# Kernel optimization log

Hardware: AMD Instinct MI355X
Metric: run time of the kernel (lower is better)

Reference implementation:

```python
import jax, jax.numpy as jnp
import numpy as np

HID, PROJ, ATTN = 512, 1024, 128
B, L = 4, 2048


def _apply_rope(x):
    # x: [B, L, 2, ATTN]; RoPE over sequence dim (axis=1)
    half = x.shape[-1] // 2
    inv_freq = jnp.power(10000.0, -jnp.arange(half, dtype=jnp.float32) / half)
    pos = jnp.arange(x.shape[1], dtype=x.dtype)
    sinusoid = pos[:, None] * inv_freq.astype(x.dtype)          # [L, half]
    sin = jnp.sin(sinusoid)[None, :, None, :]                   # [1, L, 1, half]
    cos = jnp.cos(sinusoid)[None, :, None, :]
    x1, x2 = jnp.split(x, 2, axis=-1)
    return jnp.concatenate([x1 * cos - x2 * sin, x2 * cos + x1 * sin], axis=-1)


def setup_inputs() -> dict:
    key = jax.random.key(0)
    ks = jax.random.split(key, 8)
    node = jax.random.normal(ks[0], (B, L, HID), dtype=jnp.float32)
    bias = jax.random.normal(ks[1], (B, L, L), dtype=jnp.float32)
    scaling = jnp.full((1,), ATTN ** -0.5, dtype=jnp.float32)
    w1 = jax.random.normal(ks[2], (HID, 2 * PROJ + ATTN), dtype=jnp.float32) * (HID ** -0.5)
    b1 = jnp.zeros((2 * PROJ + ATTN,), dtype=jnp.float32)
    ms_weight = jax.random.normal(ks[3], (2, ATTN), dtype=jnp.float32) * 0.02
    ms_bias = jnp.zeros((2, ATTN), dtype=jnp.float32)
    w2 = jax.random.normal(ks[4], (PROJ, HID), dtype=jnp.float32) * (PROJ ** -0.5)
    b2 = jnp.zeros((HID,), dtype=jnp.float32)
    return {"node": node, "bias": bias, "scaling": scaling, "w1": w1, "b1": b1,
            "ms_weight": ms_weight, "ms_bias": ms_bias, "w2": w2, "b2": b2}


def reference(node, bias, scaling, w1, b1, ms_weight, ms_bias, w2, b2):
    # gated projection + SiLU
    gva = jax.nn.silu(node @ w1 + b1)                           # [B, L, 2P+A]
    gates, values, base = jnp.split(gva, [PROJ, 2 * PROJ], axis=-1)
    # multi-headed scaling -> [B, L, 2, A], then RoPE, then split q/k
    qk = base[..., None, :] * ms_weight + ms_bias               # [B, L, 2, A]
    qk = _apply_rope(qk)
    q, k = qk[..., 0, :], qk[..., 1, :]                         # [B, L, A]
    logits = jnp.einsum('bid,bjd->bij', q * scaling, k) + bias  # [B, L, L]
    attn = jax.nn.softmax(logits, axis=-1)
    out = jnp.einsum('bij,bjd->bid', attn, values)              # [B, L, P]
    return (out * gates) @ w2 + b2                              # [B, L, HID]
```

## Files before the change

kernel.cpp:

```cpp
#include <hip/hip_runtime.h>
#include <math.h>

#define HIDN 512
#define PROJ 1024
#define ATTN 128
#define BATCH 4
#define SEQ 2048
#define N1 (2*PROJ+ATTN)
#define ROWS (BATCH*SEQ)

typedef __attribute__((ext_vector_type(4))) float f32x4;
typedef __attribute__((ext_vector_type(8))) short bf16x8;

__device__ __forceinline__ short f2bf(float x){
    unsigned u = __builtin_bit_cast(unsigned, x);
    unsigned rounding = 0x7fffu + ((u >> 16) & 1u);
    u += rounding;
    return (short)(u >> 16);
}
__device__ __forceinline__ float bf2f(short s){
    unsigned u = ((unsigned)(unsigned short)s) << 16;
    return __builtin_bit_cast(float, u);
}

__device__ __forceinline__ void gload16(const void* g, void* l){
    __builtin_amdgcn_global_load_lds((const __attribute__((address_space(1))) void*)g,
                                     (__attribute__((address_space(3))) void*)l,
                                     16, 0, 0);
}

template<int BK, class Epi>
__device__ __forceinline__ void gemm_bt_tile(const short* __restrict__ A, int lda,
                                             const short* __restrict__ BT, int ldb,
                                             int m0, int n0, int K, Epi epi)
{
    __shared__ __align__(16) short lA[2][128*BK];
    __shared__ __align__(16) short lB[2][128*BK];
    const int t = threadIdx.x;
    const int lane = t & 63;
    const int w = t >> 6;
    const int wr = (w >> 1) * 64, wc = (w & 1) * 64;
    const int half = lane >> 4, l16 = lane & 15;
    constexpr int SPT = BK/16;

    f32x4 acc[4][4];
    #pragma unroll
    for (int i=0;i<4;i++)
        #pragma unroll
        for (int j=0;j<4;j++)
            acc[i][j] = (f32x4){0.f,0.f,0.f,0.f};

    auto stage = [&](int buf, int k0){
        #pragma unroll
        for (int i = 0; i < SPT; i++) {
            int li = i*256 + t;
            int r = li / (BK/8), s = li % (BK/8);
            int ss = (BK==64) ? (s ^ (r & 7)) : (s ^ ((r >> 1) & 3));
            gload16(A + (size_t)(m0+r)*lda + k0 + ss*8, lA[buf] + li*8);
        }
        #pragma unroll
        for (int i = 0; i < SPT; i++) {
            int li = i*256 + t;
            int r = li / (BK/8), s = li % (BK/8);
            int ss = (BK==64) ? (s ^ (r & 7)) : (s ^ ((r >> 1) & 3));
            gload16(BT + (size_t)(n0+r)*ldb + k0 + ss*8, lB[buf] + li*8);
        }
    };

    stage(0, 0);
    __syncthreads();
    int cur = 0;
    for (int k0 = BK; k0 <= K; k0 += BK) {
        if (k0 < K) stage(cur^1, k0);
        #pragma unroll
        for (int kk = 0; kk < BK; kk += 32) {
            bf16x8 af[4], bfr[4];
            const int cs = (kk >> 3) + half;
            #pragma unroll
            for (int i=0;i<4;i++){
                int row = wr + i*16 + l16;
                int sl = (BK==64) ? (cs ^ (row & 7)) : (cs ^ ((row >> 1) & 3));
                af[i] = *(const bf16x8*)(lA[cur] + row*BK + sl*8);
            }
            #pragma unroll
            for (int j=0;j<4;j++){
                int row = wc + j*16 + l16;
                int sl = (BK==64) ? (cs ^ (row & 7)) : (cs ^ ((row >> 1) & 3));
                bfr[j] = *(const bf16x8*)(lB[cur] + row*BK + sl*8);
            }
            #pragma unroll
            for (int i=0;i<4;i++)
                #pragma unroll
                for (int j=0;j<4;j++)
                    acc[i][j] = __builtin_amdgcn_mfma_f32_16x16x32_bf16(af[i], bfr[j], acc[i][j], 0, 0, 0);
        }
        __syncthreads();
        cur ^= 1;
    }
    #pragma unroll
    for (int i=0;i<4;i++)
        #pragma unroll
        for (int j=0;j<4;j++)
            #pragma unroll
            for (int q=0;q<4;q++)
                epi(m0 + wr + i*16 + half*4 + q, n0 + wc + j*16 + l16, acc[i][j][q]);
}

template<class Epi>
__device__ __forceinline__ void gemm_bt_tile256(const short* __restrict__ A, int lda,
                                                const short* __restrict__ BT, int ldb,
                                                int m0, int n0, int K, Epi epi)
{
    constexpr int BK = 32;
    __shared__ __align__(16) short lA[2][256*BK];
    __shared__ __align__(16) short lB[2][128*BK];
    const int t = threadIdx.x;
    const int lane = t & 63;
    const int w = t >> 6;
    const int wr = (w >> 1) * 64;
    const int wc = (w & 1) * 64;
    const int half = lane >> 4, l16 = lane & 15;

    f32x4 acc[4][4];
    #pragma unroll
    for (int i=0;i<4;i++)
        #pragma unroll
        for (int j=0;j<4;j++)
            acc[i][j] = (f32x4){0.f,0.f,0.f,0.f};

    auto stage = [&](int buf, int k0){
        #pragma unroll
        for (int i = 0; i < 2; i++) {
            int li = i*512 + t;
            int r = li >> 2, s = li & 3;
            int ss = s ^ ((r >> 1) & 3);
            gload16(A + (size_t)(m0+r)*lda + k0 + ss*8, lA[buf] + li*8);
        }
        {
            int li = t;
            int r = li >> 2, s = li & 3;
            int ss = s ^ ((r >> 1) & 3);
            gload16(BT + (size_t)(n0+r)*ldb + k0 + ss*8, lB[buf] + li*8);
        }
    };

    stage(0, 0);
    __syncthreads();
    int cur = 0;
    for (int k0 = BK; k0 <= K; k0 += BK) {
        if (k0 < K) stage(cur^1, k0);
        {
            bf16x8 af[4], bfr[4];
            const int cs = half;
            #pragma unroll
            for (int i=0;i<4;i++){
                int row = wr + i*16 + l16;
                af[i] = *(const bf16x8*)(lA[cur] + row*BK + (cs ^ ((row >> 1) & 3))*8);
            }
            #pragma unroll
            for (int j=0;j<4;j++){
                int row = wc + j*16 + l16;
                bfr[j] = *(const bf16x8*)(lB[cur] + row*BK + (cs ^ ((row >> 1) & 3))*8);
            }
            #pragma unroll
            for (int i=0;i<4;i++)
                #pragma unroll
                for (int j=0;j<4;j++)
                    acc[i][j] = __builtin_amdgcn_mfma_f32_16x16x32_bf16(af[i], bfr[j], acc[i][j], 0, 0, 0);
        }
        __syncthreads();
        cur ^= 1;
    }
    #pragma unroll
    for (int i=0;i<4;i++)
        #pragma unroll
        for (int j=0;j<4;j++)
            #pragma unroll
            for (int q=0;q<4;q++)
                epi(m0 + wr + i*16 + half*4 + q, n0 + wc + j*16 + l16, acc[i][j][q]);
}

__global__ void k_cast_node(const float* __restrict__ in, short* __restrict__ out){
    int idx = blockIdx.x*256 + threadIdx.x;
    const float4 v = ((const float4*)in)[idx];
    short4 o; o.x = f2bf(v.x); o.y = f2bf(v.y); o.z = f2bf(v.z); o.w = f2bf(v.w);
    ((short4*)out)[idx] = o;
}

__global__ void k_transpose_cast(const float* __restrict__ in, short* __restrict__ out,
                                 int R, int C){
    __shared__ short tile[64][65];
    int r0 = blockIdx.y*64, c0 = blockIdx.x*64;
    int t = threadIdx.x;
    #pragma unroll
    for (int i=0;i<16;i++){
        int lin = i*256 + t; int r = lin>>6, c = lin&63;
        tile[r][c] = f2bf(in[(size_t)(r0+r)*C + c0+c]);
    }
    __syncthreads();
    #pragma unroll
    for (int i=0;i<16;i++){
        int lin = i*256 + t; int c = lin>>6, r = lin&63;
        out[(size_t)(c0+c)*R + r0+r] = tile[r][c];
    }
}

__global__ void k_transpose_v(const short* __restrict__ values, short* __restrict__ VT){
    __shared__ short tile[64][65];
    int z = blockIdx.z;
    int c0 = blockIdx.x*64, r0 = blockIdx.y*64;
    int t = threadIdx.x;
    #pragma unroll
    for (int i=0;i<16;i++){
        int lin = i*256 + t; int r = lin>>6, c = lin&63;
        tile[r][c] = values[(size_t)(z*SEQ + r0+r)*PROJ + c0+c];
    }
    __syncthreads();
    #pragma unroll
    for (int i=0;i<16;i++){
        int lin = i*256 + t; int c = lin>>6, r = lin&63;
        VT[((size_t)z*PROJ + c0+c)*SEQ + r0+r] = tile[r][c];
    }
}

__global__ __launch_bounds__(512) void k_mm1(const short* __restrict__ nodeb,
        const short* __restrict__ w1T, const float* __restrict__ b1,
        short* __restrict__ gates, short* __restrict__ values){
    int b = blockIdx.x;
    int wg = (b & 7) * 64 + (b >> 3);
    int n0 = (wg & 15) * 128;
    int m0 = (wg >> 4) * 256;
    short* dst = (n0 < PROJ) ? gates : values;
    const int coff = (n0 < PROJ) ? 0 : PROJ;
    gemm_bt_tile256(nodeb, HIDN, w1T, HIDN, m0, n0, HIDN,
        [=](int row, int col, float v){
            v += b1[col];
            v = v / (1.f + __expf(-v));
            dst[(size_t)row*PROJ + (col - coff)] = f2bf(v);
        });
}

__global__ __launch_bounds__(256) void k_mmbase(const short* __restrict__ nodeb,
        const short* __restrict__ w1T, const float* __restrict__ b1,
        short* __restrict__ baseb){
    int m0 = blockIdx.x * 128;
    const short* BT = w1T + (size_t)(2*PROJ)*HIDN;
    gemm_bt_tile<32>(nodeb, HIDN, BT, HIDN, m0, 0, HIDN,
        [=](int row, int col, float v){
            v += b1[2*PROJ + col];
            v = v / (1.f + __expf(-v));
            baseb[(size_t)row*ATTN + col] = f2bf(v);
        });
}

__global__ void k_rope2(const short* __restrict__ baseb, const float* __restrict__ msw,
                        const float* __restrict__ msb, const float* __restrict__ scaling,
                        short* __restrict__ qb, short* __restrict__ kb){
    int idx = blockIdx.x*256 + threadIdx.x;
    int d = idx & 63;
    int row = idx >> 6;
    int l = row & (SEQ-1);
    float inv = exp2f(-(float)d * (13.287712379549449f/64.f));
    float ang = (float)l * inv;
    float s = sinf(ang), c = cosf(ang);
    const short* bp = baseb + (size_t)row*ATTN;
    float b_lo = bf2f(bp[d]), b_hi = bf2f(bp[d+64]);
    float x1q = b_lo*msw[d]        + msb[d];
    float x2q = b_hi*msw[d+64]     + msb[d+64];
    float x1k = b_lo*msw[128+d]    + msb[128+d];
    float x2k = b_hi*msw[128+d+64] + msb[128+d+64];
    float sc = scaling[0];
    qb[(size_t)row*ATTN + d]    = f2bf((x1q*c - x2q*s)*sc);
    qb[(size_t)row*ATTN + d+64] = f2bf((x2q*c + x1q*s)*sc);
    kb[(size_t)row*ATTN + d]    = f2bf(x1k*c - x2k*s);
    kb[(size_t)row*ATTN + d+64] = f2bf(x2k*c + x1k*s);
}

__global__ __launch_bounds__(256) void k_qksm(
        const short* __restrict__ qg, const short* __restrict__ kg,
        const float* __restrict__ bias, short* __restrict__ P,
        float* __restrict__ lsum16)
{
    __shared__ __align__(16) short smem[32768];
    __shared__ float sl[2][128];

    const int b = blockIdx.x;
    const int wg = (b & 7) * 128 + (b >> 3);
    const int z  = wg >> 8;
    const int qt = (wg >> 4) & 15;
    const int kt = wg & 15;
    const int q0 = qt * 128, kv0 = kt * 128;

    const int t = threadIdx.x;
    const int lane = t & 63, w = t >> 6;
    const int wr = (w >> 1)*64, wc = (w & 1)*64;
    const int half = lane >> 4, l16 = lane & 15;

    const short* Kg = kg + ((size_t)z*SEQ + kv0)*ATTN;
    const short* Qg = qg + ((size_t)z*SEQ + q0)*ATTN;

    #pragma unroll
    for (int i = 0; i < 8; i++) {
        int li = i*256 + t;
        int r = li >> 4, s = li & 15;
        int ss = s ^ (r & 15);
        gload16(Kg + (size_t)r*ATTN + ss*8, smem + li*8);
        gload16(Qg + (size_t)r*ATTN + ss*8, smem + 16384 + li*8);
    }

    f32x4 acc[4][4];
    #pragma unroll
    for (int i=0;i<4;i++)
        #pragma unroll
        for (int j=0;j<4;j++)
            acc[i][j] = *(const f32x4*)(bias
                + ((size_t)z*SEQ + q0 + wc + j*16 + l16)*SEQ
                + kv0 + wr + i*16 + half*4);

    __syncthreads();

    #pragma unroll
    for (int kk = 0; kk < 128; kk += 32) {
        const int cs = (kk >> 3) + half;
        bf16x8 af[4], bfr[4];
        #pragma unroll
        for (int i=0;i<4;i++){
            int row = wr + i*16 + l16;
            af[i] = *(const bf16x8*)(smem + row*128 + (cs ^ (row & 15))*8);
        }
        #pragma unroll
        for (int j=0;j<4;j++){
            int row = wc + j*16 + l16;
            bfr[j] = *(const bf16x8*)(smem + 16384 + row*128 + (cs ^ (row & 15))*8);
        }
        #pragma unroll
        for (int i=0;i<4;i++)
            #pragma unroll
            for (int j=0;j<4;j++)
                acc[i][j] = __builtin_amdgcn_mfma_f32_16x16x32_bf16(af[i], bfr[j], acc[i][j], 0, 0, 0);
    }

    __syncthreads();

    short* pt = smem;
    float tsum[4];
    #pragma unroll
    for (int j=0;j<4;j++){
        int col = wc + j*16 + l16;
        float sj = 0.f;
        #pragma unroll
        for (int i=0;i<4;i++){
            float p0=__expf(acc[i][j][0]), p1=__expf(acc[i][j][1]);
            float p2=__expf(acc[i][j][2]), p3=__expf(acc[i][j][3]);
            sj += p0+p1+p2+p3;
            short4 pv; pv.x=f2bf(p0); pv.y=f2bf(p1); pv.z=f2bf(p2); pv.w=f2bf(p3);
            *(short4*)(pt + col*136 + wr + i*16 + half*4) = pv;
        }
        tsum[j] = sj;
    }
    #pragma unroll
    for (int j=0;j<4;j++){
        tsum[j] += __shfl_xor(tsum[j],16,64);
        tsum[j] += __shfl_xor(tsum[j],32,64);
    }
    if (half==0){
        #pragma unroll
        for (int j=0;j<4;j++) sl[wr>>6][wc + j*16 + l16] = tsum[j];
    }
    __syncthreads();

    short* Pp = P + ((size_t)z*SEQ + q0)*SEQ + kv0;
    #pragma unroll
    for (int i=0;i<8;i++){
        int idx = i*256 + t;
        int q = idx >> 4, g = idx & 15;
        *(bf16x8*)(Pp + (size_t)q*SEQ + g*8) = *(const bf16x8*)(pt + q*136 + g*8);
    }
    if (t < 128)
        lsum16[(size_t)kt*ROWS + (size_t)z*SEQ + q0 + t] = sl[0][t] + sl[1][t];
}

__global__ void k_combine(const float* __restrict__ lsum16, float* __restrict__ linv){
    int r = blockIdx.x*256 + threadIdx.x;
    float s = 0.f;
    #pragma unroll
    for (int kt=0; kt<16; kt++) s += lsum16[(size_t)kt*ROWS + r];
    linv[r] = 1.f/s;
}

__global__ __launch_bounds__(256) void k_pv2(const short* __restrict__ P,
        const short* __restrict__ VT, const short* __restrict__ gates,
        const float* __restrict__ linv, short* __restrict__ a2){
    int b = blockIdx.x;
    int wg = (b & 7) * 64 + (b >> 3);
    int xx = wg & 7, yy = (wg >> 3) & 15, z = wg >> 7;
    const short* A = P  + (size_t)z*SEQ*SEQ;
    const short* B = VT + (size_t)z*PROJ*SEQ;
    int n0 = xx*128, m0 = yy*128;
    gemm_bt_tile<64>(A, SEQ, B, SEQ, m0, n0, SEQ,
        [=](int r, int c, float v){
            size_t ri = (size_t)z*SEQ + r;
            size_t gi = ri*PROJ + c;
            a2[gi] = f2bf(v * linv[ri] * bf2f(gates[gi]));
        });
}

__global__ __launch_bounds__(256) void k_mm2(const short* __restrict__ a2,
        const short* __restrict__ w2T, const float* __restrict__ b2,
        float* __restrict__ out){
    int b = blockIdx.x;
    int wg = (b & 7) * 32 + (b >> 3);
    int n0 = (wg & 3)*128, m0 = (wg >> 2)*128;
    gemm_bt_tile<32>(a2, PROJ, w2T, PROJ, m0, n0, PROJ,
        [=](int r, int c, float v){
            out[(size_t)r*HIDN + c] = v + b2[c];
        });
}

extern "C" void kernel_launch(void* const* d_in, const int* in_sizes, int n_in,
                              void* d_out, int out_size, void* d_ws, size_t ws_size,
                              hipStream_t stream) {
    const float* node    = (const float*)d_in[0];
    const float* bias    = (const float*)d_in[1];
    const float* scaling = (const float*)d_in[2];
    const float* w1      = (const float*)d_in[3];
    const float* b1      = (const float*)d_in[4];
    const float* msw     = (const float*)d_in[5];
    const float* msb     = (const float*)d_in[6];
    const float* w2      = (const float*)d_in[7];
    const float* b2      = (const float*)d_in[8];
    float* out = (float*)d_out;

    char* p = (char*)d_ws;
    auto alloc = [&](size_t bytes){ char* r = p; p += (bytes + 255) & ~(size_t)255; return r; };
    short* nodeb  = (short*)alloc((size_t)ROWS*HIDN*2);
    short* w1T    = (short*)alloc((size_t)N1*HIDN*2);
    short* w2T    = (short*)alloc((size_t)HIDN*PROJ*2);
    short* gates  = (short*)alloc((size_t)ROWS*PROJ*2);
    short* values = (short*)alloc((size_t)ROWS*PROJ*2);
    short* VT     = (short*)alloc((size_t)BATCH*PROJ*SEQ*2);
    short* baseb  = (short*)alloc((size_t)ROWS*ATTN*2);
    short* qb     = (short*)alloc((size_t)ROWS*ATTN*2);
    short* kb     = (short*)alloc((size_t)ROWS*ATTN*2);
    short* Pbuf   = (short*)alloc((size_t)BATCH*SEQ*SEQ*2);
    float* lsum16 = (float*)alloc((size_t)16*ROWS*4);
    float* linv   = (float*)alloc((size_t)ROWS*4);
    short* a2buf  = (short*)alloc((size_t)ROWS*PROJ*2);

    k_cast_node<<<ROWS*HIDN/1024, 256, 0, stream>>>(node, nodeb);
    k_transpose_cast<<<dim3(N1/64, HIDN/64), 256, 0, stream>>>(w1, w1T, HIDN, N1);
    k_transpose_cast<<<dim3(HIDN/64, PROJ/64), 256, 0, stream>>>(w2, w2T, PROJ, HIDN);
    k_mm1<<<16*(ROWS/256), 512, 0, stream>>>(nodeb, w1T, b1, gates, values);
    k_mmbase<<<ROWS/128, 256, 0, stream>>>(nodeb, w1T, b1, baseb);
    k_transpose_v<<<dim3(PROJ/64, SEQ/64, BATCH), 256, 0, stream>>>(values, VT);
    k_rope2<<<ROWS*64/256, 256, 0, stream>>>(baseb, msw, msb, scaling, qb, kb);
    k_qksm<<<16*16*BATCH, 256, 0, stream>>>(qb, kb, bias, Pbuf, lsum16);
    k_combine<<<ROWS/256, 256, 0, stream>>>(lsum16, linv);
    k_pv2<<<(PROJ/128)*(SEQ/128)*BATCH, 256, 0, stream>>>(Pbuf, VT, gates, linv, a2buf);
    k_mm2<<<(HIDN/128)*(ROWS/128), 256, 0, stream>>>(a2buf, w2T, b2, out);
}
```

Before: 148.5 us.

## Fuse values transpose into mm1 epilogue with LDS-staged coalesced stores

The first GEMM's epilogue now stages its bf16 output tile in shared memory. For value columns it writes the tile transposed straight into VT, so the separate transpose kernel and the intermediate values buffer are no longer needed. Gate outputs are also staged and written as 16-byte vector stores instead of scattered 2-byte stores. This removes one kernel launch and a full read plus write of the values tensor, at the cost of extra LDS traffic and barriers in the epilogue.

```diff
diff --git a/kernel.cpp b/kernel.cpp
--- a/kernel.cpp
+++ b/kernel.cpp
@@ -106,80 +106,6 @@
                 epi(m0 + wr + i*16 + half*4 + q, n0 + wc + j*16 + l16, acc[i][j][q]);
 }
 
-template<class Epi>
-__device__ __forceinline__ void gemm_bt_tile256(const short* __restrict__ A, int lda,
-                                                const short* __restrict__ BT, int ldb,
-                                                int m0, int n0, int K, Epi epi)
-{
-    constexpr int BK = 32;
-    __shared__ __align__(16) short lA[2][256*BK];
-    __shared__ __align__(16) short lB[2][128*BK];
-    const int t = threadIdx.x;
-    const int lane = t & 63;
-    const int w = t >> 6;
-    const int wr = (w >> 1) * 64;
-    const int wc = (w & 1) * 64;
-    const int half = lane >> 4, l16 = lane & 15;
-
-    f32x4 acc[4][4];
-    #pragma unroll
-    for (int i=0;i<4;i++)
-        #pragma unroll
-        for (int j=0;j<4;j++)
-            acc[i][j] = (f32x4){0.f,0.f,0.f,0.f};
-
-    auto stage = [&](int buf, int k0){
-        #pragma unroll
-        for (int i = 0; i < 2; i++) {
-            int li = i*512 + t;
-            int r = li >> 2, s = li & 3;
-            int ss = s ^ ((r >> 1) & 3);
-            gload16(A + (size_t)(m0+r)*lda + k0 + ss*8, lA[buf] + li*8);
-        }
-        {
-            int li = t;
-            int r = li >> 2, s = li & 3;
-            int ss = s ^ ((r >> 1) & 3);
-            gload16(BT + (size_t)(n0+r)*ldb + k0 + ss*8, lB[buf] + li*8);
-        }
-    };
-
-    stage(0, 0);
-    __syncthreads();
-    int cur = 0;
-    for (int k0 = BK; k0 <= K; k0 += BK) {
-        if (k0 < K) stage(cur^1, k0);
-        {
-            bf16x8 af[4], bfr[4];
-            const int cs = half;
-            #pragma unroll
-            for (int i=0;i<4;i++){
-                int row = wr + i*16 + l16;
-                af[i] = *(const bf16x8*)(lA[cur] + row*BK + (cs ^ ((row >> 1) & 3))*8);
-            }
-            #pragma unroll
-            for (int j=0;j<4;j++){
-                int row = wc + j*16 + l16;
-                bfr[j] = *(const bf16x8*)(lB[cur] + row*BK + (cs ^ ((row >> 1) & 3))*8);
-            }
-            #pragma unroll
-            for (int i=0;i<4;i++)
-                #pragma unroll
-                for (int j=0;j<4;j++)
-                    acc[i][j] = __builtin_amdgcn_mfma_f32_16x16x32_bf16(af[i], bfr[j], acc[i][j], 0, 0, 0);
-        }
-        __syncthreads();
-        cur ^= 1;
-    }
-    #pragma unroll
-    for (int i=0;i<4;i++)
-        #pragma unroll
-        for (int j=0;j<4;j++)
-            #pragma unroll
-            for (int q=0;q<4;q++)
-                epi(m0 + wr + i*16 + half*4 + q, n0 + wc + j*16 + l16, acc[i][j][q]);
-}
-
 __global__ void k_cast_node(const float* __restrict__ in, short* __restrict__ out){
     int idx = blockIdx.x*256 + threadIdx.x;
     const float4 v = ((const float4*)in)[idx];
@@ -205,39 +131,113 @@
     }
 }
 
-__global__ void k_transpose_v(const short* __restrict__ values, short* __restrict__ VT){
-    __shared__ short tile[64][65];
-    int z = blockIdx.z;
-    int c0 = blockIdx.x*64, r0 = blockIdx.y*64;
-    int t = threadIdx.x;
-    #pragma unroll
-    for (int i=0;i<16;i++){
-        int lin = i*256 + t; int r = lin>>6, c = lin&63;
-        tile[r][c] = values[(size_t)(z*SEQ + r0+r)*PROJ + c0+c];
-    }
-    __syncthreads();
-    #pragma unroll
-    for (int i=0;i<16;i++){
-        int lin = i*256 + t; int c = lin>>6, r = lin&63;
-        VT[((size_t)z*PROJ + c0+c)*SEQ + r0+r] = tile[r][c];
-    }
-}
-
 __global__ __launch_bounds__(512) void k_mm1(const short* __restrict__ nodeb,
         const short* __restrict__ w1T, const float* __restrict__ b1,
-        short* __restrict__ gates, short* __restrict__ values){
-    int b = blockIdx.x;
-    int wg = (b & 7) * 64 + (b >> 3);
-    int n0 = (wg & 15) * 128;
-    int m0 = (wg >> 4) * 256;
-    short* dst = (n0 < PROJ) ? gates : values;
-    const int coff = (n0 < PROJ) ? 0 : PROJ;
-    gemm_bt_tile256(nodeb, HIDN, w1T, HIDN, m0, n0, HIDN,
-        [=](int row, int col, float v){
-            v += b1[col];
-            v = v / (1.f + __expf(-v));
-            dst[(size_t)row*PROJ + (col - coff)] = f2bf(v);
-        });
+        short* __restrict__ gates, short* __restrict__ VT){
+    __shared__ __align__(16) short smem[24576];
+    short* lA = smem;
+    short* lB = smem + 16384;
+
+    const int b = blockIdx.x;
+    const int wg = (b & 7) * 64 + (b >> 3);
+    const int n0 = (wg & 15) * 128;
+    const int m0 = (wg >> 4) * 256;
+    const int t = threadIdx.x;
+    const int lane = t & 63;
+    const int w = t >> 6;
+    const int wr = (w >> 1) * 64, wc = (w & 1) * 64;
+    const int half = lane >> 4, l16 = lane & 15;
+
+    f32x4 acc[4][4];
+    #pragma unroll
+    for (int i=0;i<4;i++)
+        #pragma unroll
+        for (int j=0;j<4;j++)
+            acc[i][j] = (f32x4){0.f,0.f,0.f,0.f};
+
+    auto stage = [&](int buf, int k0){
+        #pragma unroll
+        for (int i = 0; i < 2; i++) {
+            int li = i*512 + t;
+            int r = li >> 2, s = li & 3;
+            int ss = s ^ ((r >> 1) & 3);
+            gload16(nodeb + (size_t)(m0+r)*HIDN + k0 + ss*8, lA + buf*8192 + li*8);
+        }
+        {
+            int li = t;
+            int r = li >> 2, s = li & 3;
+            int ss = s ^ ((r >> 1) & 3);
+            gload16(w1T + (size_t)(n0+r)*HIDN + k0 + ss*8, lB + buf*4096 + li*8);
+        }
+    };
+
+    stage(0, 0);
+    __syncthreads();
+    int cur = 0;
+    for (int k0 = 32; k0 <= HIDN; k0 += 32) {
+        if (k0 < HIDN) stage(cur^1, k0);
+        {
+            bf16x8 af[4], bfr[4];
+            const int cs = half;
+            #pragma unroll
+            for (int i=0;i<4;i++){
+                int row = wr + i*16 + l16;
+                af[i] = *(const bf16x8*)(lA + cur*8192 + row*32 + (cs ^ ((row >> 1) & 3))*8);
+            }
+            #pragma unroll
+            for (int j=0;j<4;j++){
+                int row = wc + j*16 + l16;
+                bfr[j] = *(const bf16x8*)(lB + cur*4096 + row*32 + (cs ^ ((row >> 1) & 3))*8);
+            }
+            #pragma unroll
+            for (int i=0;i<4;i++)
+                #pragma unroll
+                for (int j=0;j<4;j++)
+                    acc[i][j] = __builtin_amdgcn_mfma_f32_16x16x32_bf16(af[i], bfr[j], acc[i][j], 0, 0, 0);
+        }
+        __syncthreads();
+        cur ^= 1;
+    }
+
+    const bool isv = (n0 >= PROJ);
+    const int z = m0 >> 11, m0b = m0 & (SEQ-1);
+    float bcol[4];
+    #pragma unroll
+    for (int j=0;j<4;j++) bcol[j] = b1[n0 + wc + j*16 + l16];
+
+    #pragma unroll
+    for (int p = 0; p < 2; ++p){
+        if ((wr >> 7) == p){
+            const int rbase = wr - p*128;
+            #pragma unroll
+            for (int i=0;i<4;i++)
+                #pragma unroll
+                for (int j=0;j<4;j++){
+                    const int c = wc + j*16 + l16;
+                    #pragma unroll
+                    for (int q=0;q<4;q++){
+                        int r = rbase + i*16 + half*4 + q;
+                        float v = acc[i][j][q] + bcol[j];
+                        v = v / (1.f + __expf(-v));
+                        short bv = f2bf(v);
+                        if (isv) smem[c*136 + r] = bv;
+                        else     smem[r*136 + c] = bv;
+                    }
+                }
+        }
+        __syncthreads();
+        #pragma unroll
+        for (int it=0; it<4; ++it){
+            int idx = it*512 + t;
+            int rr = idx >> 4, g = idx & 15;
+            bf16x8 v = *(const bf16x8*)(smem + rr*136 + g*8);
+            if (isv)
+                *(bf16x8*)(VT + ((size_t)z*PROJ + (n0 - PROJ) + rr)*SEQ + m0b + p*128 + g*8) = v;
+            else
+                *(bf16x8*)(gates + (size_t)(m0 + p*128 + rr)*PROJ + n0 + g*8) = v;
+        }
+        __syncthreads();
+    }
 }
 
 __global__ __launch_bounds__(256) void k_mmbase(const short* __restrict__ nodeb,
@@ -437,7 +437,6 @@
     short* w1T    = (short*)alloc((size_t)N1*HIDN*2);
     short* w2T    = (short*)alloc((size_t)HIDN*PROJ*2);
     short* gates  = (short*)alloc((size_t)ROWS*PROJ*2);
-    short* values = (short*)alloc((size_t)ROWS*PROJ*2);
     short* VT     = (short*)alloc((size_t)BATCH*PROJ*SEQ*2);
     short* baseb  = (short*)alloc((size_t)ROWS*ATTN*2);
     short* qb     = (short*)alloc((size_t)ROWS*ATTN*2);
@@ -450,9 +449,8 @@
     k_cast_node<<<ROWS*HIDN/1024, 256, 0, stream>>>(node, nodeb);
     k_transpose_cast<<<dim3(N1/64, HIDN/64), 256, 0, stream>>>(w1, w1T, HIDN, N1);
     k_transpose_cast<<<dim3(HIDN/64, PROJ/64), 256, 0, stream>>>(w2, w2T, PROJ, HIDN);
-    k_mm1<<<16*(ROWS/256), 512, 0, stream>>>(nodeb, w1T, b1, gates, values);
+    k_mm1<<<16*(ROWS/256), 512, 0, stream>>>(nodeb, w1T, b1, gates, VT);
     k_mmbase<<<ROWS/128, 256, 0, stream>>>(nodeb, w1T, b1, baseb);
-    k_transpose_v<<<dim3(PROJ/64, SEQ/64, BATCH), 256, 0, stream>>>(values, VT);
     k_rope2<<<ROWS*64/256, 256, 0, stream>>>(baseb, msw, msb, scaling, qb, kb);
     k_qksm<<<16*16*BATCH, 256, 0, stream>>>(qb, kb, bias, Pbuf, lsum16);
     k_combine<<<ROWS/256, 256, 0, stream>>>(lsum16, linv);
```

New measurement: 160.5 us. +8.1%, slower.
